# Optimization experiments

Hardware: AMD Instinct MI355X
Metric: run time of the kernel (lower is better)

The kernel has to match this reference:

```python
import jax, jax.numpy as jnp
import numpy as np

B, DIN, NU, N, ORDER = 256, 64, 256, 207, 3
KC = (ORDER + 1) * (DIN + NU)  # 1280 concat channels into gate conv
SQRT_D = float(np.sqrt(NU))


def layer_norm(x, w, b, eps=1e-5):
    mu = jnp.mean(x, -1, keepdims=True)
    var = jnp.mean((x - mu) ** 2, -1, keepdims=True)
    return (x - mu) / jnp.sqrt(var + eps) * w + b


def spatial_diffusion(x, adj, order):
    # x: (B, C, N). Order-K diffusion with self term, matching SpatialConvOrderK:
    # x_k[..., w] = sum_v adj[w, v] * x_{k-1}[..., v]
    outs = [x]
    xk = x
    for _ in range(order):
        xk = jnp.einsum('bcv,wv->bcw', xk, adj)
        outs.append(xk)
    return jnp.concatenate(outs, axis=1)  # (B, (order+1)*C, N)


def transformer_layer(s, in_proj_w, in_proj_b, out_proj_w, out_proj_b,
                      ln1_w, ln1_b, ln2_w, ln2_b, ffn_w1, ffn_b1, ffn_w2, ffn_b2):
    # s: (N, B, d). Single-head post-LN TransformerEncoderLayer, eval mode (dropout off).
    qkv = s @ in_proj_w.T + in_proj_b
    q, k, v = jnp.split(qkv, 3, axis=-1)
    attn = jax.nn.softmax(jnp.einsum('nbd,mbd->bnm', q, k) / SQRT_D, axis=-1)
    o = jnp.einsum('bnm,mbd->nbd', attn, v) @ out_proj_w.T + out_proj_b
    s = layer_norm(s + o, ln1_w, ln1_b)
    f = jax.nn.relu(s @ ffn_w1.T + ffn_b1) @ ffn_w2.T + ffn_b2
    return layer_norm(s + f, ln2_w, ln2_b)


def gcgru_forward(x, delta_t, h, adj, mask_last_tp, embed,
                  in_proj_w, in_proj_b, out_proj_w, out_proj_b,
                  ln1_w, ln1_b, ln2_w, ln2_b, ffn_w1, ffn_b1, ffn_w2, ffn_b2,
                  W_u, b_u, W_c, b_c, step):
    if step != 0:
        h_p = jnp.transpose(h, (2, 0, 1))  # (N, B, NU)
        inp = h_p + embed[:, None, :] * jnp.transpose(mask_last_tp, (2, 0, 1))  # (N,B,1) bcast
        eps = jnp.tanh(transformer_layer(inp, in_proj_w, in_proj_b, out_proj_w, out_proj_b,
                                         ln1_w, ln1_b, ln2_w, ln2_b,
                                         ffn_w1, ffn_b1, ffn_w2, ffn_b2))
        eps = jnp.transpose(eps, (1, 2, 0))  # (B, NU, N)
        dt = delta_t[..., None]  # (B, 1, 1)
        h = jnp.sqrt(1.0 - dt) * h - jnp.sqrt(dt) * eps
    xg = jnp.concatenate([x, h], axis=1)  # (B, DIN+NU, N)
    # update_gate and c_gate receive the identical concat -> compute diffusion once
    z = spatial_diffusion(xg, adj, ORDER)  # (B, KC, N)
    u = jax.nn.sigmoid(jnp.einsum('bcn,oc->bon', z, W_u) + b_u[None, :, None])
    c = jnp.tanh(jnp.einsum('bcn,oc->bon', z, W_c) + b_c[None, :, None])
    return u * h + (1.0 - u) * c


def setup_inputs() -> dict:
    key = jax.random.key(0)
    ks = jax.random.split(key, 16)
    d = NU

    def nrm(k, shape, s=0.02):
        return jax.random.normal(k, shape, jnp.float32) * s

    return dict(
        x=jax.random.normal(ks[0], (B, DIN, N), jnp.float32),
        delta_t=jax.random.uniform(ks[1], (B, 1), jnp.float32, 0.01, 0.99),
        h=jax.random.normal(ks[2], (B, NU, N), jnp.float32),
        adj=jax.random.uniform(ks[3], (N, N), jnp.float32) / N,
        mask=jnp.ones((B, 1, N), jnp.float32),
        mask_last_tp=(jax.random.uniform(ks[4], (B, 1, N)) > 0.5).astype(jnp.float32),
        time_encoding=jnp.zeros((B, d), jnp.float32),
        step=1,
        embed=nrm(ks[5], (N, d), 1.0),
        in_proj_w=nrm(ks[6], (3 * d, d)), in_proj_b=jnp.zeros((3 * d,), jnp.float32),
        out_proj_w=nrm(ks[7], (d, d)), out_proj_b=jnp.zeros((d,), jnp.float32),
        ln1_w=jnp.ones((d,), jnp.float32), ln1_b=jnp.zeros((d,), jnp.float32),
        ln2_w=jnp.ones((d,), jnp.float32), ln2_b=jnp.zeros((d,), jnp.float32),
        ffn_w1=nrm(ks[8], (d, d)), ffn_b1=jnp.zeros((d,), jnp.float32),
        ffn_w2=nrm(ks[9], (d, d)), ffn_b2=jnp.zeros((d,), jnp.float32),
        W_u=nrm(ks[10], (NU, KC)), b_u=jnp.zeros((NU,), jnp.float32),
        W_c=nrm(ks[11], (NU, KC)), b_c=jnp.zeros((NU,), jnp.float32),
    )


def reference(x, delta_t, h, adj, mask, mask_last_tp, time_encoding, step,
              embed, in_proj_w, in_proj_b, out_proj_w, out_proj_b,
              ln1_w, ln1_b, ln2_w, ln2_b, ffn_w1, ffn_b1, ffn_w2, ffn_b2,
              W_u, b_u, W_c, b_c):
    # mask / time_encoding are accepted but unused, exactly as in the torch epsilon.forward
    return gcgru_forward(x, delta_t, h, adj, mask_last_tp, embed,
                         in_proj_w, in_proj_b, out_proj_w, out_proj_b,
                         ln1_w, ln1_b, ln2_w, ln2_b, ffn_w1, ffn_b1, ffn_w2, ffn_b2,
                         W_u, b_u, W_c, b_c, step)
```

## Files before the change

kernel.cpp:

```cpp
#include <hip/hip_runtime.h>
#include <hip/hip_bf16.h>

typedef __hip_bfloat16 bf16;
typedef __attribute__((ext_vector_type(8))) short s8v;
typedef __attribute__((ext_vector_type(4))) short s4v;
typedef __attribute__((ext_vector_type(4))) float f4v;

#define MFMA(a, b, c) __builtin_amdgcn_mfma_f32_16x16x32_bf16(a, b, c, 0, 0, 0)

#define B_    256
#define DIN_  64
#define NU_   256
#define NN_   207
#define KC_   1280
#define NB_   (NN_ * B_)
#define NBD_  13565952LL

#define WU_OFF   0LL
#define WC_OFF   327680LL
#define IP_OFF   655360LL
#define OP_OFF   851968LL
#define F1_OFF   917504LL
#define F2_OFF   983040LL
#define ADJ_OFF  1048576LL
#define WEXT_N   (ADJ_OFF + 207LL * 256LL)

__device__ __forceinline__ float bf2f(bf16 v) { return __bfloat162float(v); }
__device__ __forceinline__ bf16  f2bf(float v) { return __float2bfloat16(v); }
__device__ __forceinline__ short f2s(float v) { bf16 t = __float2bfloat16(v); return *(short*)&t; }

__device__ __forceinline__ void gl16(const void* g, void* l) {
    __builtin_amdgcn_global_load_lds(
        (const __attribute__((address_space(1))) void*)g,
        (__attribute__((address_space(3))) void*)l, 16, 0, 0);
}

#define SWZ(rr, cb) ((rr) * 64 + ((((cb) + q) ^ ((rr) & 7)) << 3))

__global__ __launch_bounds__(256) void cvt_w_k(
    const float* __restrict__ Wu, const float* __restrict__ Wc,
    const float* __restrict__ ip, const float* __restrict__ op,
    const float* __restrict__ f1, const float* __restrict__ f2,
    const float* __restrict__ adj, short* __restrict__ dst)
{
    long long t = (long long)blockIdx.x * 256 + threadIdx.x;
    long long nt = (long long)gridDim.x * 256;
    for (long long g = t; g < 262144; g += nt) {
        long long e = g * 4;
        const float* src; long long off;
        if (e < WC_OFF)      { src = Wu; off = e; }
        else if (e < IP_OFF) { src = Wc; off = e - WC_OFF; }
        else if (e < OP_OFF) { src = ip; off = e - IP_OFF; }
        else if (e < F1_OFF) { src = op; off = e - OP_OFF; }
        else if (e < F2_OFF) { src = f1; off = e - F1_OFF; }
        else                 { src = f2; off = e - F2_OFF; }
        float4 fv = *(const float4*)(src + off);
        s4v v = {f2s(fv.x), f2s(fv.y), f2s(fv.z), f2s(fv.w)};
        *(s4v*)(dst + e) = v;
    }
    short* adst = dst + ADJ_OFF;
    for (long long g = t; g < 207LL * 256LL; g += nt) {
        int r = (int)(g >> 8), c = (int)(g & 255);
        adst[g] = (c < NN_) ? f2s(adj[r * NN_ + c]) : (short)0;
    }
}

template<int EPI>
__global__ __launch_bounds__(512) void gemm_pipe(
    const short* __restrict__ A, int lda,
    const short* __restrict__ Wb, int ldb,
    const float* __restrict__ bias, bf16* __restrict__ C, int ldc,
    int K, int act, short* __restrict__ vt,
    const float* __restrict__ bu, const float* __restrict__ bc,
    const bf16* __restrict__ hnT, float* __restrict__ outF)
{
    __shared__ __align__(16) short As[2][256 * 64];
    __shared__ __align__(16) short Bs[2][256 * 64];
    const int w_ = blockIdx.y * gridDim.x + blockIdx.x;
    const int nswz = gridDim.x;
    const int xr = w_ & 7, sidx = w_ >> 3;
    const int mt = xr + 8 * (sidx / nswz);
    const int nt = sidx % nswz;
    if (mt >= 207) return;
    const int m0 = mt * 256, n0 = nt * 256;
    const int tid = threadIdx.x;
    const int lane = tid & 63, wid = tid >> 6;
    const int l15 = lane & 15, q = lane >> 4;
    const int wm = (wid >> 2) * 128, wn = (wid & 3) * 64;
    const int seg_r = lane >> 3;
    const int csw8 = ((lane & 7) ^ seg_r) << 3;
    const int nk = K >> 6;

    const short* ap[4];
    const short* bp[4];
#pragma unroll
    for (int i = 0; i < 4; i++) {
        int gm = m0 + (wid * 4 + i) * 8 + seg_r;
        ap[i] = A + (long long)gm * lda + csw8;
        int gn = n0 + (wid * 4 + i) * 8 + seg_r;
        int pr = EPI ? ((gn & 1) * 256 + (gn >> 1)) : gn;
        bp[i] = Wb + (long long)pr * ldb + csw8;
    }
    int offA[8], offB[4];
#pragma unroll
    for (int i = 0; i < 8; i++)
        offA[i] = (wm + i * 16 + l15) * 64 + ((q ^ (l15 & 7)) << 3);
#pragma unroll
    for (int j = 0; j < 4; j++)
        offB[j] = (wn + j * 16 + l15) * 64 + ((q ^ (l15 & 7)) << 3);

    f4v acc[8][4] = {};

    auto stage = [&](int k0, int pb) {
#pragma unroll
        for (int i = 0; i < 4; i++) {
            gl16(ap[i] + k0, &As[pb][(wid * 4 + i) * 512]);
            gl16(bp[i] + k0, &Bs[pb][(wid * 4 + i) * 512]);
        }
    };

    stage(0, 0);
    int cur = 0;
    for (int t = 0; t < nk; ++t) {
        asm volatile("s_waitcnt vmcnt(0)" ::: "memory");
        __builtin_amdgcn_s_barrier();
        __builtin_amdgcn_sched_barrier(0);
        if (t + 1 < nk) stage((t + 1) << 6, cur ^ 1);
        const short* Asp = &As[cur][0];
        const short* Bsp = &Bs[cur][0];
#pragma unroll
        for (int cs = 0; cs < 2; ++cs) {
            const int cx = cs << 5;
            s8v bfv[4];
#pragma unroll
            for (int j = 0; j < 4; j++) bfv[j] = *(const s8v*)&Bsp[offB[j] ^ cx];
#pragma unroll
            for (int half = 0; half < 2; ++half) {
                s8v af[4];
#pragma unroll
                for (int i = 0; i < 4; i++) af[i] = *(const s8v*)&Asp[offA[half * 4 + i] ^ cx];
                __builtin_amdgcn_s_setprio(1);
#pragma unroll
                for (int i = 0; i < 4; i++)
#pragma unroll
                    for (int j = 0; j < 4; j++)
                        acc[half * 4 + i][j] = MFMA(af[i], bfv[j], acc[half * 4 + i][j]);
                __builtin_amdgcn_s_setprio(0);
            }
        }
        cur ^= 1;
    }

    if (EPI == 0) {
#pragma unroll
        for (int i = 0; i < 8; i++) {
            int mbase = m0 + wm + i * 16 + q * 4;
#pragma unroll
            for (int j = 0; j < 4; j++) {
                int n = n0 + wn + j * 16 + l15;
                float bv = bias ? bias[n] : 0.f;
#pragma unroll
                for (int r = 0; r < 4; r++) {
                    int m = mbase + r;
                    float v = acc[i][j][r] + bv;
                    if (act == 3) v = fmaxf(v, 0.f);
                    if (vt && n >= 512) {
                        int d = n - 512;
                        int bb = m / NN_;
                        int node = m - bb * NN_;
                        vt[((long long)bb * 256 + d) * 208 + node] = f2s(v);
                    } else {
                        C[(long long)m * ldc + n] = f2bf(v);
                    }
                }
            }
        }
    } else {
#pragma unroll
        for (int i = 0; i < 8; i++) {
            int mbase = m0 + wm + i * 16 + q * 4;
#pragma unroll
            for (int j = 0; j < 4; j++) {
                int n = n0 + wn + j * 16 + l15;
                int och = n >> 1;
                float bv = (n & 1) ? bc[och] : bu[och];
#pragma unroll
                for (int r = 0; r < 4; r++) {
                    int m = mbase + r;
                    float pre = acc[i][j][r] + bv;
                    float oth = __shfl_xor(pre, 1);
                    if (!(n & 1)) {
                        float u = 1.f / (1.f + __expf(-pre));
                        float cg = tanhf(oth);
                        float hv = bf2f(hnT[(long long)m * 256 + och]);
                        int bb = m / NN_;
                        int node = m - bb * NN_;
                        outF[((long long)bb * NU_ + och) * NN_ + node] = u * hv + (1.f - u) * cg;
                    }
                }
            }
        }
    }
}

__global__ __launch_bounds__(256) void gemm_nk0(
    const short* __restrict__ A, int lda,
    const float* __restrict__ Wf, int ldb,
    const float* __restrict__ bias, bf16* __restrict__ C, int ldc,
    int M, int N, int K, int act, short* __restrict__ vt)
{
    __shared__ __align__(16) short As[2][128 * 64];
    __shared__ __align__(16) short Bs[2][128 * 64];
    const int tid = threadIdx.x;
    const int lane = tid & 63, wid = tid >> 6;
    const int l15 = lane & 15, q = lane >> 4;
    const int wm = (wid >> 1) * 64, wn = (wid & 1) * 64;
    const int m0 = blockIdx.y * 128, n0 = blockIdx.x * 128;

    f4v acc[4][4] = {};
    const int nk = K >> 6;

    auto stage = [&](int k0, int pb) {
#pragma unroll
        for (int i = 0; i < 4; i++) {
            int idx = tid + (i << 8);
            int r = idx >> 3, c = idx & 7;
            int gm = m0 + r, gk = k0 + (c << 3);
            s8v v = {0, 0, 0, 0, 0, 0, 0, 0};
            if (gm < M) v = *(const s8v*)(A + (long long)gm * lda + gk);
            *(s8v*)&As[pb][r * 64 + ((c ^ (r & 7)) << 3)] = v;
        }
#pragma unroll
        for (int i = 0; i < 8; i++) {
            int idx = tid + (i << 8);
            int r = idx >> 4, c4 = idx & 15;
            int gn = n0 + r, gk = k0 + (c4 << 2);
            s4v v = {0, 0, 0, 0};
            if (gn < N) {
                float4 fx = *(const float4*)(Wf + (long long)gn * ldb + gk);
                v[0] = f2s(fx.x); v[1] = f2s(fx.y); v[2] = f2s(fx.z); v[3] = f2s(fx.w);
            }
            *(s4v*)&Bs[pb][r * 64 + (((c4 >> 1) ^ (r & 7)) << 3) + ((c4 & 1) << 2)] = v;
        }
    };

    stage(0, 0);
    __syncthreads();
    int pp = 0;
    for (int t = 0; t < nk; ++t) {
        if (t + 1 < nk) stage((t + 1) << 6, pp ^ 1);
#pragma unroll
        for (int ks = 0; ks < 64; ks += 32) {
            const int cb = ks >> 3;
            s8v af[4], bfv[4];
#pragma unroll
            for (int i = 0; i < 4; i++) {
                int rr = wm + i * 16 + l15;
                af[i] = *(const s8v*)&As[pp][SWZ(rr, cb)];
            }
#pragma unroll
            for (int j = 0; j < 4; j++) {
                int rr = wn + j * 16 + l15;
                bfv[j] = *(const s8v*)&Bs[pp][SWZ(rr, cb)];
            }
#pragma unroll
            for (int i = 0; i < 4; i++)
#pragma unroll
                for (int j = 0; j < 4; j++)
                    acc[i][j] = MFMA(af[i], bfv[j], acc[i][j]);
        }
        __syncthreads();
        pp ^= 1;
    }

#pragma unroll
    for (int i = 0; i < 4; i++) {
        int mbase = m0 + wm + i * 16 + q * 4;
#pragma unroll
        for (int j = 0; j < 4; j++) {
            int n = n0 + wn + j * 16 + l15;
            if (n >= N) continue;
            float bv = bias ? bias[n] : 0.f;
#pragma unroll
            for (int r = 0; r < 4; r++) {
                int m = mbase + r;
                if (m >= M) continue;
                float v = acc[i][j][r] + bv;
                if (act == 3) v = fmaxf(v, 0.f);
                if (vt && n >= 512) {
                    int d = n - 512;
                    int bb = m / NN_;
                    int node = m - bb * NN_;
                    vt[((long long)bb * 256 + d) * 208 + node] = f2s(v);
                } else {
                    C[(long long)m * ldc + n] = f2bf(v);
                }
            }
        }
    }
}

__global__ __launch_bounds__(256) void attn_k(
    const short* __restrict__ qk, const short* __restrict__ vt,
    bf16* __restrict__ ao)
{
    __shared__ __align__(16) short Plds[64 * 232];
    __shared__ float sums[64];
    const int tid = threadIdx.x;
    const int lane = tid & 63, w = tid >> 6;
    const int l15 = lane & 15, quad = lane >> 4;
    const int w_ = blockIdx.y * gridDim.x + blockIdx.x;
    const int xr = w_ & 7, sidx = w_ >> 3;
    const int b = xr + 8 * (sidx >> 2);
    const int q0 = (sidx & 3) * 64;
    const long long rowcap = (long long)NB_ - 1;

    long long qrow = (long long)b * NN_ + q0 + w * 16 + l15;
    if (qrow > rowcap) qrow = rowcap;
    const short* qp = qk + qrow * 512;
    s8v bq[8];
#pragma unroll
    for (int ks = 0; ks < 8; ks++)
        bq[ks] = *(const s8v*)(qp + ks * 32 + quad * 8);

    const short* jp[13];
#pragma unroll
    for (int jf = 0; jf < 13; jf++) {
        long long jrow = (long long)b * NN_ + jf * 16 + l15;
        if (jrow > rowcap) jrow = rowcap;
        jp[jf] = qk + jrow * 512 + 256;
    }

    f4v sacc[13] = {};
#pragma unroll
    for (int ks = 0; ks < 8; ks++) {
        const int off = ks * 32 + quad * 8;
#pragma unroll
        for (int jf = 0; jf < 13; jf++) {
            s8v a = *(const s8v*)(jp[jf] + off);
            sacc[jf] = MFMA(a, bq[ks], sacc[jf]);
        }
    }

    float mx = -3.0e38f;
    float pv[13][4];
#pragma unroll
    for (int jf = 0; jf < 13; jf++)
#pragma unroll
        for (int r = 0; r < 4; r++) {
            int j = jf * 16 + quad * 4 + r;
            float v = (j < NN_) ? sacc[jf][r] * 0.0625f : -3.0e38f;
            pv[jf][r] = v;
            mx = fmaxf(mx, v);
        }
    mx = fmaxf(mx, __shfl_xor(mx, 16));
    mx = fmaxf(mx, __shfl_xor(mx, 32));
    float sum = 0.f;
#pragma unroll
    for (int jf = 0; jf < 13; jf++)
#pragma unroll
        for (int r = 0; r < 4; r++) {
            float p = __expf(pv[jf][r] - mx);
            pv[jf][r] = p;
            sum += p;
        }
    sum += __shfl_xor(sum, 16);
    sum += __shfl_xor(sum, 32);

    const int qloc = w * 16 + l15;
#pragma unroll
    for (int jf = 0; jf < 13; jf++)
#pragma unroll
        for (int r = 0; r < 4; r++)
            Plds[qloc * 232 + jf * 16 + quad * 4 + r] = f2s(pv[jf][r]);
    if (quad == 0) sums[qloc] = 1.f / sum;
#pragma unroll
    for (int i = 0; i < 4; i++) {
        int u = tid + i * 256;
        Plds[(u >> 4) * 232 + 208 + (u & 15)] = 0;
    }
    __syncthreads();

    const short* vbase = vt + (long long)b * 256 * 208;
    f4v oacc[16] = {};
#pragma unroll
    for (int ks = 0; ks < 7; ks++) {
        s8v pa = *(const s8v*)&Plds[(w * 16 + l15) * 232 + ks * 32 + quad * 8];
#pragma unroll
        for (int df = 0; df < 16; df++) {
            s8v vb = *(const s8v*)(vbase + (df * 16 + l15) * 208 + ks * 32 + quad * 8);
            oacc[df] = MFMA(pa, vb, oacc[df]);
        }
    }

#pragma unroll
    for (int df = 0; df < 16; df++) {
        int d = df * 16 + l15;
#pragma unroll
        for (int r = 0; r < 4; r++) {
            int ql = w * 16 + quad * 4 + r;
            int qg = q0 + ql;
            if (qg < NN_)
                ao[((long long)b * NN_ + qg) * 256 + d] = f2bf(oacc[df][r] * sums[ql]);
        }
    }
}

template<int WB>
__global__ __launch_bounds__(256) void diff_k(
    const float* __restrict__ adj, const short* __restrict__ adjb,
    const short* __restrict__ zT_in,
    short* __restrict__ zT_out, int col_in, int col_out)
{
    __shared__ __align__(16) short As[2][128 * 64];
    __shared__ __align__(16) short Bs[2][128 * 64];
    const int tid = threadIdx.x;
    const int lane = tid & 63, wid = tid >> 6;
    const int l15 = lane & 15, q = lane >> 4;
    const int wm = (wid >> 1) * 64, wn = (wid & 1) * 64;
    const int m0 = blockIdx.y * 128, n0 = blockIdx.x * 128;
    const long long zb = (long long)blockIdx.z * NN_ * KC_;
    const int seg_r = lane >> 3, chunk = lane & 7;
    const int csw8 = (chunk ^ seg_r) << 3;
    const int bv_ = tid & 63, bcg = tid >> 6;

    f4v acc[4][4] = {};

    auto stageA = [&](int k0, int pb) {
        if (WB) {
#pragma unroll
            for (int i = 0; i < 4; i++) {
                int seg = wid * 4 + i;
                int gm = m0 + seg * 8 + seg_r;
                if (gm > NN_ - 1) gm = NN_ - 1;
                gl16(adjb + gm * 256 + k0 + csw8, &As[pb][seg * 512]);
            }
        } else {
#pragma unroll
            for (int i = 0; i < 32; i++) {
                int idx = tid + (i << 8);
                int r = idx >> 6, c = idx & 63;
                int gm = m0 + r, gk = k0 + c;
                short vv = (gm < NN_ && gk < NN_) ? f2s(adj[gm * NN_ + gk]) : (short)0;
                As[pb][r * 64 + (((c >> 3) ^ (r & 7)) << 3) + (c & 7)] = vv;
            }
        }
    };
    auto loadB = [&](int k0, s8v* breg) {
#pragma unroll
        for (int i = 0; i < 4; i++) {
            int gv = k0 + bv_, gc = n0 + (bcg + i * 4) * 8;
            s8v val = {0, 0, 0, 0, 0, 0, 0, 0};
            if (gv < NN_ && gc < 320)
                val = *(const s8v*)&zT_in[zb + (long long)gv * KC_ + col_in + gc];
            breg[i] = val;
        }
    };
    auto writeB = [&](s8v* breg, int pb) {
#pragma unroll
        for (int i = 0; i < 4; i++) {
            int cg = bcg + i * 4;
#pragma unroll
            for (int e = 0; e < 8; e++) {
                int row = cg * 8 + e;
                Bs[pb][row * 64 + (((bv_ >> 3) ^ (row & 7)) << 3) + (bv_ & 7)] = breg[i][e];
            }
        }
    };

    s8v breg[4];
    loadB(0, breg);
    stageA(0, 0);
    writeB(breg, 0);
    __syncthreads();
    int pp = 0;
    for (int t = 0; t < 4; ++t) {
        if (t < 3) { loadB((t + 1) << 6, breg); stageA((t + 1) << 6, pp ^ 1); }
#pragma unroll
        for (int ks = 0; ks < 64; ks += 32) {
            const int cb = ks >> 3;
            s8v af[4], bfv[4];
#pragma unroll
            for (int i = 0; i < 4; i++) {
                int rr = wm + i * 16 + l15;
                af[i] = *(const s8v*)&As[pp][SWZ(rr, cb)];
            }
#pragma unroll
            for (int j = 0; j < 4; j++) {
                int rr = wn + j * 16 + l15;
                bfv[j] = *(const s8v*)&Bs[pp][SWZ(rr, cb)];
            }
#pragma unroll
            for (int i = 0; i < 4; i++)
#pragma unroll
                for (int j = 0; j < 4; j++)
                    acc[i][j] = MFMA(af[i], bfv[j], acc[i][j]);
        }
        if (t < 3) writeB(breg, pp ^ 1);
        __syncthreads();
        pp ^= 1;
    }

#pragma unroll
    for (int i = 0; i < 4; i++) {
        int mbase = m0 + wm + i * 16 + q * 4;
#pragma unroll
        for (int j = 0; j < 4; j++) {
            int n = n0 + wn + j * 16 + l15;
            if (n >= 320) continue;
#pragma unroll
            for (int r = 0; r < 4; r++) {
                int m = mbase + r;
                if (m >= NN_) continue;
                zT_out[zb + (long long)m * KC_ + col_out + n] = f2s(acc[i][j][r]);
            }
        }
    }
}

__global__ __launch_bounds__(256) void gates_k0(
    const short* __restrict__ zT, const float* __restrict__ Wu,
    const float* __restrict__ Wc, const float* __restrict__ bu,
    const float* __restrict__ bc, const bf16* __restrict__ hnT,
    float* __restrict__ out)
{
    __shared__ __align__(16) short As[2][128 * 64];
    __shared__ __align__(16) short Bu[2][64 * 64];
    __shared__ __align__(16) short Bc[2][64 * 64];
    const int tid = threadIdx.x;
    const int lane = tid & 63, wid = tid >> 6;
    const int l15 = lane & 15, q = lane >> 4;
    const int b = blockIdx.z;
    const int m0 = blockIdx.y * 128;
    const int n0 = blockIdx.x * 64;
    const long long zb = (long long)b * NN_ * KC_;

    f4v aU[2][4] = {}, aC[2][4] = {};

    auto stage = [&](int k0, int pb) {
#pragma unroll
        for (int i = 0; i < 4; i++) {
            int idx = tid + (i << 8);
            int r = idx >> 3, c = idx & 7;
            int gw = m0 + r;
            s8v v = {0, 0, 0, 0, 0, 0, 0, 0};
            if (gw < NN_) v = *(const s8v*)&zT[zb + (long long)gw * KC_ + k0 + (c << 3)];
            *(s8v*)&As[pb][r * 64 + ((c ^ (r & 7)) << 3)] = v;
        }
#pragma unroll
        for (int i = 0; i < 4; i++) {
            int idx = tid + (i << 8);
            int r = idx >> 4, c4 = idx & 15;
            long long widx = (long long)(n0 + r) * KC_ + k0 + (c4 << 2);
            float4 fu = *(const float4*)(Wu + widx);
            float4 fc = *(const float4*)(Wc + widx);
            s4v vu = {f2s(fu.x), f2s(fu.y), f2s(fu.z), f2s(fu.w)};
            s4v vc = {f2s(fc.x), f2s(fc.y), f2s(fc.z), f2s(fc.w)};
            int di = r * 64 + (((c4 >> 1) ^ (r & 7)) << 3) + ((c4 & 1) << 2);
            *(s4v*)&Bu[pb][di] = vu;
            *(s4v*)&Bc[pb][di] = vc;
        }
    };

    stage(0, 0);
    __syncthreads();
    int pp = 0;
    for (int t = 0; t < 20; ++t) {
        if (t < 19) stage((t + 1) << 6, pp ^ 1);
#pragma unroll
        for (int ks = 0; ks < 64; ks += 32) {
            const int cb = ks >> 3;
            s8v af[2], bfu[4], bfc[4];
#pragma unroll
            for (int i = 0; i < 2; i++) {
                int rr = wid * 32 + i * 16 + l15;
                af[i] = *(const s8v*)&As[pp][SWZ(rr, cb)];
            }
#pragma unroll
            for (int j = 0; j < 4; j++) {
                int rr = j * 16 + l15;
                bfu[j] = *(const s8v*)&Bu[pp][SWZ(rr, cb)];
                bfc[j] = *(const s8v*)&Bc[pp][SWZ(rr, cb)];
            }
#pragma unroll
            for (int i = 0; i < 2; i++)
#pragma unroll
                for (int j = 0; j < 4; j++) {
                    aU[i][j] = MFMA(af[i], bfu[j], aU[i][j]);
                    aC[i][j] = MFMA(af[i], bfc[j], aC[i][j]);
                }
        }
        __syncthreads();
        pp ^= 1;
    }

#pragma unroll
    for (int i = 0; i < 2; i++) {
        int wbase = m0 + wid * 32 + i * 16 + q * 4;
#pragma unroll
        for (int j = 0; j < 4; j++) {
            int och = n0 + j * 16 + l15;
            float bvu = bu[och];
            float bvc = bc[och];
#pragma unroll
            for (int r = 0; r < 4; r++) {
                int w = wbase + r;
                if (w >= NN_) continue;
                float u = 1.f / (1.f + __expf(-(aU[i][j][r] + bvu)));
                float cg = tanhf(aC[i][j][r] + bvc);
                float hv = bf2f(hnT[((long long)b * NN_ + w) * 256 + och]);
                out[((long long)b * NU_ + och) * NN_ + w] = u * hv + (1.f - u) * cg;
            }
        }
    }
}

__global__ __launch_bounds__(256) void build_inp_k(
    const float* __restrict__ h, const float* __restrict__ embed,
    const float* __restrict__ mlt, bf16* __restrict__ inp)
{
    __shared__ float t[32][33];
    const int b = blockIdx.z;
    const int n0 = blockIdx.x * 32, c0 = blockIdx.y * 32;
    const int t5 = threadIdx.x & 31, t8 = threadIdx.x >> 5;
#pragma unroll
    for (int r = 0; r < 4; r++) {
        int c = c0 + t8 + r * 8;
        int n = n0 + t5;
        t[t8 + r * 8][t5] = (n < NN_) ? h[((long long)b * 256 + c) * NN_ + n] : 0.f;
    }
    __syncthreads();
#pragma unroll
    for (int r = 0; r < 4; r++) {
        int n = n0 + t8 + r * 8;
        int c = c0 + t5;
        if (n < NN_) {
            float v = t[t5][t8 + r * 8] + embed[n * 256 + c] * mlt[b * NN_ + n];
            inp[((long long)b * NN_ + n) * 256 + c] = f2bf(v);
        }
    }
}

__global__ __launch_bounds__(256) void add_ln_k(
    const bf16* __restrict__ xr, const bf16* __restrict__ yr,
    const float* __restrict__ w, const float* __restrict__ bb,
    bf16* __restrict__ out, int do_tanh)
{
    const int lane = threadIdx.x & 63, wv = threadIdx.x >> 6;
    const long long row = (long long)blockIdx.x * 4 + wv;
    const long long base = row * 256 + lane * 4;
    s4v xv = *(const s4v*)((const short*)xr + base);
    s4v yv = *(const s4v*)((const short*)yr + base);
    float v[4];
    float sum = 0.f;
#pragma unroll
    for (int i = 0; i < 4; i++) {
        short sx = xv[i], sy = yv[i];
        v[i] = bf2f(*(bf16*)&sx) + bf2f(*(bf16*)&sy);
        sum += v[i];
    }
#pragma unroll
    for (int s = 1; s < 64; s <<= 1) sum += __shfl_xor(sum, s);
    float mu = sum * (1.f / 256.f);
    float vs = 0.f;
#pragma unroll
    for (int i = 0; i < 4; i++) { float d = v[i] - mu; vs += d * d; }
#pragma unroll
    for (int s = 1; s < 64; s <<= 1) vs += __shfl_xor(vs, s);
    float inv = rsqrtf(vs * (1.f / 256.f) + 1e-5f);
    s4v ov;
#pragma unroll
    for (int i = 0; i < 4; i++) {
        float r = (v[i] - mu) * inv * w[lane * 4 + i] + bb[lane * 4 + i];
        if (do_tanh) r = tanhf(r);
        ov[i] = f2s(r);
    }
    *(s4v*)((short*)out + base) = ov;
}

__global__ __launch_bounds__(256) void hnew_k(
    const float* __restrict__ h, const bf16* __restrict__ epsb,
    const float* __restrict__ dt, const int* __restrict__ step, bf16* __restrict__ hnT)
{
    __shared__ float t[32][33];
    const int b = blockIdx.z;
    const int n0 = blockIdx.x * 32, c0 = blockIdx.y * 32;
    const int t5 = threadIdx.x & 31, t8 = threadIdx.x >> 5;
#pragma unroll
    for (int r = 0; r < 4; r++) {
        int c = c0 + t8 + r * 8;
        int n = n0 + t5;
        t[t8 + r * 8][t5] = (n < NN_) ? h[((long long)b * 256 + c) * NN_ + n] : 0.f;
    }
    __syncthreads();
    const int st = *step;
    const float d = dt[b];
    const float sa = sqrtf(fmaxf(1.f - d, 0.f)), sb = sqrtf(d);
#pragma unroll
    for (int r = 0; r < 4; r++) {
        int n = n0 + t8 + r * 8;
        int c = c0 + t5;
        if (n < NN_) {
            float hv = t[t5][t8 + r * 8];
            float val = hv;
            if (st != 0) {
                float ev = bf2f(epsb[((long long)b * NN_ + n) * 256 + c]);
                val = sa * hv - sb * ev;
            }
            hnT[((long long)b * NN_ + n) * 256 + c] = f2bf(val);
        }
    }
}

__global__ __launch_bounds__(256) void zx_k(
    const float* __restrict__ x, short* __restrict__ zT)
{
    __shared__ float t[32][33];
    const int b = blockIdx.z;
    const int n0 = blockIdx.x * 32, c0 = blockIdx.y * 32;
    const int t5 = threadIdx.x & 31, t8 = threadIdx.x >> 5;
#pragma unroll
    for (int r = 0; r < 4; r++) {
        int c = c0 + t8 + r * 8;
        int n = n0 + t5;
        t[t8 + r * 8][t5] = (n < NN_) ? x[((long long)b * DIN_ + c) * NN_ + n] : 0.f;
    }
    __syncthreads();
#pragma unroll
    for (int r = 0; r < 4; r++) {
        int n = n0 + t8 + r * 8;
        int c = c0 + t5;
        if (n < NN_)
            zT[((long long)b * NN_ + n) * KC_ + c] = f2s(t[t5][t8 + r * 8]);
    }
}

__global__ __launch_bounds__(256) void zcopy_k(
    const short* __restrict__ hnT, short* __restrict__ zT)
{
    long long u = (long long)blockIdx.x * 256 + threadIdx.x;
    long long row = u >> 5;
    int cu = (int)(u & 31);
    s8v v = *(const s8v*)(hnT + row * 256 + cu * 8);
    *(s8v*)(zT + row * KC_ + 64 + cu * 8) = v;
}

extern "C" void kernel_launch(void* const* d_in, const int* in_sizes, int n_in,
                              void* d_out, int out_size, void* d_ws, size_t ws_size,
                              hipStream_t stream) {
    const float* x          = (const float*)d_in[0];
    const float* delta_t    = (const float*)d_in[1];
    const float* h          = (const float*)d_in[2];
    const float* adj        = (const float*)d_in[3];
    const float* mlt        = (const float*)d_in[5];
    const int*  step        = (const int*)d_in[7];
    const float* embed      = (const float*)d_in[8];
    const float* in_proj_w  = (const float*)d_in[9];
    const float* in_proj_b  = (const float*)d_in[10];
    const float* out_proj_w = (const float*)d_in[11];
    const float* out_proj_b = (const float*)d_in[12];
    const float* ln1_w      = (const float*)d_in[13];
    const float* ln1_b      = (const float*)d_in[14];
    const float* ln2_w      = (const float*)d_in[15];
    const float* ln2_b      = (const float*)d_in[16];
    const float* ffn_w1     = (const float*)d_in[17];
    const float* ffn_b1     = (const float*)d_in[18];
    const float* ffn_w2     = (const float*)d_in[19];
    const float* ffn_b2     = (const float*)d_in[20];
    const float* W_u        = (const float*)d_in[21];
    const float* b_u        = (const float*)d_in[22];
    const float* W_c        = (const float*)d_in[23];
    const float* b_c        = (const float*)d_in[24];
    float* out = (float*)d_out;
    bf16* ws   = (bf16*)d_ws;

    bf16* inp = ws;
    short* qk = (short*)(ws + 1 * NBD_);
    short* vt = (short*)(ws + 3 * NBD_);
    bf16* ao  = ws + 4 * NBD_ + 65536;
    bf16* o   = ws + 1 * NBD_;
    bf16* s   = ws + 2 * NBD_;
    bf16* f   = ws + 1 * NBD_;
    bf16* f2  = ws + 3 * NBD_;
    bf16* eps = ws + 2 * NBD_;
    bf16* hnT = ws;
    short* zT = (short*)(ws + 1 * NBD_);
    short* wext = (short*)(ws + 6 * NBD_);

    const size_t need = (size_t)(6 * NBD_ + WEXT_N) * 2;
    const bool fast = ws_size >= need;

    short* wuc  = wext + WU_OFF;
    short* ipb  = wext + IP_OFF;
    short* opb  = wext + OP_OFF;
    short* f1b  = wext + F1_OFF;
    short* f2b  = wext + F2_OFF;
    short* adjb = wext + ADJ_OFF;

    if (fast)
        cvt_w_k<<<dim3(1024), dim3(256), 0, stream>>>(
            W_u, W_c, in_proj_w, out_proj_w, ffn_w1, ffn_w2, adj, wext);

    build_inp_k<<<dim3(7, 8, 256), dim3(256), 0, stream>>>(h, embed, mlt, inp);

    if (fast)
        gemm_pipe<0><<<dim3(3, 208), dim3(512), 0, stream>>>(
            (const short*)inp, 256, ipb, 256, in_proj_b,
            (bf16*)qk, 512, 256, 0, vt, nullptr, nullptr, nullptr, nullptr);
    else
        gemm_nk0<<<dim3(6, 414), dim3(256), 0, stream>>>(
            (const short*)inp, 256, in_proj_w, 256, in_proj_b,
            (bf16*)qk, 512, NB_, 768, 256, 0, vt);

    attn_k<<<dim3(4, 256), dim3(256), 0, stream>>>(qk, vt, ao);

    if (fast)
        gemm_pipe<0><<<dim3(1, 208), dim3(512), 0, stream>>>(
            (const short*)ao, 256, opb, 256, out_proj_b,
            o, 256, 256, 0, nullptr, nullptr, nullptr, nullptr, nullptr);
    else
        gemm_nk0<<<dim3(2, 414), dim3(256), 0, stream>>>(
            (const short*)ao, 256, out_proj_w, 256, out_proj_b, o, 256, NB_, 256, 256, 0, nullptr);

    add_ln_k<<<dim3(NB_ / 4), dim3(256), 0, stream>>>(inp, o, ln1_w, ln1_b, s, 0);

    if (fast)
        gemm_pipe<0><<<dim3(1, 208), dim3(512), 0, stream>>>(
            (const short*)s, 256, f1b, 256, ffn_b1,
            f, 256, 256, 3, nullptr, nullptr, nullptr, nullptr, nullptr);
    else
        gemm_nk0<<<dim3(2, 414), dim3(256), 0, stream>>>(
            (const short*)s, 256, ffn_w1, 256, ffn_b1, f, 256, NB_, 256, 256, 3, nullptr);

    if (fast)
        gemm_pipe<0><<<dim3(1, 208), dim3(512), 0, stream>>>(
            (const short*)f, 256, f2b, 256, ffn_b2,
            f2, 256, 256, 0, nullptr, nullptr, nullptr, nullptr, nullptr);
    else
        gemm_nk0<<<dim3(2, 414), dim3(256), 0, stream>>>(
            (const short*)f, 256, ffn_w2, 256, ffn_b2, f2, 256, NB_, 256, 256, 0, nullptr);

    add_ln_k<<<dim3(NB_ / 4), dim3(256), 0, stream>>>(s, f2, ln2_w, ln2_b, eps, 1);

    hnew_k<<<dim3(7, 8, 256), dim3(256), 0, stream>>>(h, eps, delta_t, step, hnT);

    zx_k<<<dim3(7, 2, 256), dim3(256), 0, stream>>>(x, zT);
    zcopy_k<<<dim3(6624), dim3(256), 0, stream>>>((const short*)hnT, zT);

    if (fast) {
        diff_k<1><<<dim3(3, 2, 256), dim3(256), 0, stream>>>(adj, adjb, zT, zT, 0, 320);
        diff_k<1><<<dim3(3, 2, 256), dim3(256), 0, stream>>>(adj, adjb, zT, zT, 320, 640);
        diff_k<1><<<dim3(3, 2, 256), dim3(256), 0, stream>>>(adj, adjb, zT, zT, 640, 960);
    } else {
        diff_k<0><<<dim3(3, 2, 256), dim3(256), 0, stream>>>(adj, nullptr, zT, zT, 0, 320);
        diff_k<0><<<dim3(3, 2, 256), dim3(256), 0, stream>>>(adj, nullptr, zT, zT, 320, 640);
        diff_k<0><<<dim3(3, 2, 256), dim3(256), 0, stream>>>(adj, nullptr, zT, zT, 640, 960);
    }

    if (fast)
        gemm_pipe<1><<<dim3(2, 208), dim3(512), 0, stream>>>(
            zT, KC_, wuc, KC_, nullptr,
            nullptr, 0, KC_, 0, nullptr, b_u, b_c, hnT, out);
    else
        gates_k0<<<dim3(4, 2, 256), dim3(256), 0, stream>>>(
            zT, W_u, W_c, b_u, b_c, hnT, out);

    (void)in_sizes; (void)n_in; (void)out_size; (void)ws_size;
}
```

Baseline: 822.4 us.

## Split A and B tile staging to prefetch A two iterations ahead

The GEMM main loop now issues A-tile loads two K-steps ahead and B-tile loads one step ahead, instead of loading both one step ahead. It waits with a partial vmcnt so the newest A loads can still be in flight when compute starts. A second barrier per iteration guards the A buffer before it is overwritten. The aim is to hide more global-load latency behind the MFMA work, at the cost of an extra barrier in every iteration.

```diff
diff --git a/kernel.cpp b/kernel.cpp
--- a/kernel.cpp
+++ b/kernel.cpp
@@ -111,23 +111,33 @@
 
     f4v acc[8][4] = {};
 
-    auto stage = [&](int k0, int pb) {
-#pragma unroll
-        for (int i = 0; i < 4; i++) {
+    auto stageA = [&](int t) {
+        const int pb = t & 1;
+        const int k0 = t << 6;
+#pragma unroll
+        for (int i = 0; i < 4; i++)
             gl16(ap[i] + k0, &As[pb][(wid * 4 + i) * 512]);
+    };
+    auto stageB = [&](int t) {
+        const int pb = t & 1;
+        const int k0 = t << 6;
+#pragma unroll
+        for (int i = 0; i < 4; i++)
             gl16(bp[i] + k0, &Bs[pb][(wid * 4 + i) * 512]);
-        }
     };
 
-    stage(0, 0);
-    int cur = 0;
+    stageA(0);
+    stageB(0);
+    if (nk > 1) stageA(1);
+
     for (int t = 0; t < nk; ++t) {
-        asm volatile("s_waitcnt vmcnt(0)" ::: "memory");
+        if (t + 1 < nk) { asm volatile("s_waitcnt vmcnt(4)" ::: "memory"); }
+        else            { asm volatile("s_waitcnt vmcnt(0)" ::: "memory"); }
         __builtin_amdgcn_s_barrier();
         __builtin_amdgcn_sched_barrier(0);
-        if (t + 1 < nk) stage((t + 1) << 6, cur ^ 1);
-        const short* Asp = &As[cur][0];
-        const short* Bsp = &Bs[cur][0];
+        if (t + 1 < nk) stageB(t + 1);
+        const short* Asp = &As[t & 1][0];
+        const short* Bsp = &Bs[t & 1][0];
 #pragma unroll
         for (int cs = 0; cs < 2; ++cs) {
             const int cx = cs << 5;
@@ -148,7 +158,9 @@
                 __builtin_amdgcn_s_setprio(0);
             }
         }
-        cur ^= 1;
+        __builtin_amdgcn_s_barrier();
+        __builtin_amdgcn_sched_barrier(0);
+        if (t + 2 < nk) stageA(t + 2);
     }
 
     if (EPI == 0) {
```

Measured after the change: 828.6 us. No clear change (+0.8%).
